# Performance work log

Measured on AMD Instinct MI355X. Metric: run time of the kernel, lower is better.

Reference implementation:

```python
import jax, jax.numpy as jnp
import numpy as np
from jax import lax

EPS = 1e-4  # BatchNorm eps from the module
K = 3       # kernel_size
PAD = 1     # padding


def setup_inputs() -> dict:
    key = jax.random.key(0)
    k1, k2, k3 = jax.random.split(key, 3)
    N, Cin, H, Wd = 32, 256, 56, 56
    Cout = 256
    x = jax.random.normal(k1, (N, Cin, H, Wd), dtype=jnp.float32)
    gamma = jnp.ones((Cin,), dtype=jnp.float32)
    beta_bn = jnp.zeros((Cin,), dtype=jnp.float32)
    W = jax.random.normal(k2, (Cout, Cin, K, K), dtype=jnp.float32) * 0.05
    b = jax.random.normal(k3, (Cout,), dtype=jnp.float32) * 0.01
    return {"x": x, "gamma": gamma, "beta_bn": beta_bn, "W": W, "b": b}


def _conv(x, w, padding):
    return lax.conv_general_dilated(
        x, w, window_strides=(1, 1),
        padding=[(padding, padding), (padding, padding)],
        dimension_numbers=("NCHW", "OIHW", "NCHW"))


def reference(x, gamma, beta_bn, W, b):
    # BatchNorm2d in training mode: batch statistics over (N, H, W), biased var
    mu = jnp.mean(x, axis=(0, 2, 3), keepdims=True)
    var = jnp.var(x, axis=(0, 2, 3), keepdims=True)
    xn = (x - mu) * lax.rsqrt(var + EPS)
    xn = xn * gamma[None, :, None, None] + beta_bn[None, :, None, None]

    # BinActiv: per-pixel channel-mean of |x|, then sign-binarize
    m = jnp.mean(jnp.abs(xn), axis=1, keepdims=True)  # [N,1,H,W]
    xb = jnp.sign(xn)

    # Binarize weights; alpha = L1 norm per output filter / n
    n = W.shape[1] * W.shape[2] * W.shape[3]
    alpha = jnp.sum(jnp.abs(W), axis=(1, 2, 3)) / n  # [Cout]
    Wb = jnp.sign(W)

    y = _conv(xb, Wb, PAD) + b[None, :, None, None]

    # beta map: box filter (stride 1) over channel-mean magnitudes
    box = jnp.full((1, 1, K, K), 1.0 / (K * K), dtype=x.dtype)
    beta_map = _conv(m, box, PAD)  # [N,1,Ho,Wo]

    out = jax.nn.relu(y * beta_map * alpha[None, :, None, None])
    return out
```

## Files before the change

### kernel.cpp

```cpp
#include <hip/hip_runtime.h>
#include <cstdint>
#include <cstddef>

#define N_    32
#define C_    256
#define H_    56
#define W_    56
#define HW_   (H_ * W_)
#define NHW_  (N_ * HW_)
#define COUT_ 256
#define EPS_  1e-4f
#define PW_   58
#define PIMG_ (PW_ * PW_)

__global__ void k_bn_partial(const float* __restrict__ x,
                             float* __restrict__ ps, float* __restrict__ pq) {
    const int c = blockIdx.x >> 3;
    const int s = blockIdx.x & 7;
    const int t = threadIdx.x;
    float sm = 0.f, sq = 0.f;
    for (int n = s * 4; n < s * 4 + 4; ++n) {
        const float4* p = (const float4*)(x + (size_t)(n * C_ + c) * HW_);
        for (int i = t; i < HW_ / 4; i += 256) {
            float4 v = p[i];
            sm += v.x + v.y + v.z + v.w;
            sq += v.x * v.x + v.y * v.y + v.z * v.z + v.w * v.w;
        }
    }
    __shared__ float ls[256], lq[256];
    ls[t] = sm; lq[t] = sq;
    __syncthreads();
    for (int off = 128; off >= 1; off >>= 1) {
        if (t < off) { ls[t] += ls[t + off]; lq[t] += lq[t + off]; }
        __syncthreads();
    }
    if (t == 0) { ps[s * C_ + c] = ls[0]; pq[s * C_ + c] = lq[0]; }
}

__global__ void k_bn_final(const float* __restrict__ ps, const float* __restrict__ pq,
                           const float* __restrict__ gamma, const float* __restrict__ beta,
                           float* __restrict__ a, float* __restrict__ bb) {
    const int c = threadIdx.x;
    float sm = 0.f, sq = 0.f;
    for (int s = 0; s < 8; ++s) { sm += ps[s * C_ + c]; sq += pq[s * C_ + c]; }
    float mu   = sm * (1.f / NHW_);
    float var  = sq * (1.f / NHW_) - mu * mu;
    float rstd = rsqrtf(var + EPS_);
    float g    = gamma[c] * rstd;
    a[c]  = g;
    bb[c] = beta[c] - mu * g;
}

__global__ void k_wpack(const float* __restrict__ Wt, float* __restrict__ alpha,
                        uint64_t* __restrict__ wbits, int* __restrict__ ctab) {
    const int co = blockIdx.x;
    const int ci = threadIdx.x;
    const int lane = ci & 63, wave = ci >> 6;
    const float* p = Wt + (size_t)(co * C_ + ci) * 9;
    float wv[9];
    float asum = 0.f;
#pragma unroll
    for (int t = 0; t < 9; ++t) { wv[t] = p[t]; asum += fabsf(wv[t]); }
    __shared__ int Pl[9];
    if (ci < 9) Pl[ci] = 0;
    __syncthreads();
#pragma unroll
    for (int t = 0; t < 9; ++t) {
        uint64_t mask = __ballot(wv[t] > 0.f);
        if (lane == 0) {
            wbits[((size_t)wave * 9 + t) * COUT_ + co] = mask;
            atomicAdd(&Pl[t], (int)__popcll(mask));
        }
    }
    __shared__ float red[256];
    red[ci] = asum;
    __syncthreads();
    for (int off = 128; off >= 1; off >>= 1) {
        if (ci < off) red[ci] += red[ci + off];
        __syncthreads();
    }
    if (ci == 0) alpha[co] = red[0] * (1.f / 2304.f);
    if (ci < 9) {
        const int rc = ci / 3, cc = ci % 3;
        unsigned m9 = (rc == 0 ? 0x007u : 0u) | (rc == 2 ? 0x1C0u : 0u)
                    | (cc == 0 ? 0x049u : 0u) | (cc == 2 ? 0x124u : 0u);
        int s = 0;
#pragma unroll
        for (int t = 0; t < 9; ++t)
            if ((m9 >> t) & 1) s += 2 * Pl[t] - 256;
        ctab[ci * 256 + co] = s;
    }
}

__global__ void k_mpack(const float* __restrict__ x, const float* __restrict__ a,
                        const float* __restrict__ bb, uint64_t* __restrict__ xbits,
                        float* __restrict__ m) {
    const int p = blockIdx.x * 256 + threadIdx.x;
    const int wd = blockIdx.y;
    const int n = p / HW_;
    const int hw = p - n * HW_;
    const int h = hw / W_;
    const int w = hw - h * W_;
    const float* xp = x + (size_t)n * C_ * HW_ + (size_t)(wd * 64) * HW_ + hw;
    float macc = 0.f;
    uint64_t bw = 0;
#pragma unroll
    for (int j = 0; j < 64; ++j) {
        const int c = wd * 64 + j;
        float xn = fmaf(xp[(size_t)j * HW_], a[c], bb[c]);
        macc += fabsf(xn);
        bw |= (xn > 0.f) ? (1ull << j) : 0ull;
    }
    xbits[((size_t)wd * N_ + n) * PIMG_ + (size_t)(h + 1) * PW_ + (w + 1)] = bw;
    atomicAdd(&m[p], macc * (1.f / C_));
}

__global__ void k_box(const float* __restrict__ m, float* __restrict__ beta_map) {
    const int idx = blockIdx.x * 256 + threadIdx.x;
    if (idx >= NHW_) return;
    const int w = idx % W_;
    const int h = (idx / W_) % H_;
    const int n = idx / HW_;
    const float* mp = m + (size_t)n * HW_;
    float s = 0.f;
#pragma unroll
    for (int dh = 0; dh < 3; ++dh) {
        int ih = h + dh - 1;
        if (ih < 0 || ih >= H_) continue;
#pragma unroll
        for (int dw = 0; dw < 3; ++dw) {
            int iw = w + dw - 1;
            if (iw < 0 || iw >= W_) continue;
            s += mp[ih * W_ + iw];
        }
    }
    beta_map[idx] = s * (1.f / 9.f);
}

#define XNP(ACC, X64, W64) do {                                   \
    uint32_t _wl = (uint32_t)(W64), _wh = (uint32_t)((W64) >> 32); \
    uint32_t _xl = (uint32_t)(X64), _xh = (uint32_t)((X64) >> 32); \
    uint32_t _t0, _t1;                                             \
    asm("v_xor_b32 %0, %3, %5\n\t"                                 \
        "v_xor_b32 %1, %4, %6\n\t"                                 \
        "v_bcnt_u32_b32 %2, %0, %2\n\t"                            \
        "v_bcnt_u32_b32 %2, %1, %2"                                \
        : "=&v"(_t0), "=&v"(_t1), "+v"(ACC)                        \
        : "s"(_wl), "s"(_wh), "v"(_xl), "v"(_xh));                 \
} while (0)

__global__ void __launch_bounds__(256, 8)
k_conv(const uint64_t* __restrict__ xbits, const uint64_t* __restrict__ wbits,
       const int* __restrict__ ctab, const float* __restrict__ beta_map,
       const float* __restrict__ alpha, const float* __restrict__ bias,
       float* __restrict__ out) {
    const int p   = blockIdx.x * 256 + (int)threadIdx.x;
    const int grp = blockIdx.y;
    const int n  = p / HW_;
    const int hw = p - n * HW_;
    const int h  = hw / W_;
    const int w  = hw - h * W_;

    const int rowcls = (h == 0) ? 0 : ((h == H_ - 1) ? 2 : 1);
    const int colcls = (w == 0) ? 0 : ((w == W_ - 1) ? 2 : 1);
    const int* crow = ctab + (rowcls * 3 + colcls) * 256 + grp * 64;
    const float bm = beta_map[p];
    float* op = out + (size_t)n * COUT_ * HW_ + (size_t)(grp * 64) * HW_ + hw;

#pragma unroll 1
    for (int ch = 0; ch < 8; ++ch) {
        int acc[8];
#pragma unroll
        for (int i = 0; i < 8; ++i) acc[i] = 0;

#pragma unroll 1
        for (int wd = 0; wd < 4; ++wd) {
            const uint64_t* xp = xbits + ((size_t)wd * N_ + n) * PIMG_
                                       + (size_t)h * PW_ + w;
            const uint64_t* wq = wbits + (size_t)wd * 9 * COUT_ + grp * 64 + ch * 8;
#pragma unroll 3
            for (int t = 0; t < 9; ++t) {
                const uint64_t xv = *(const volatile uint64_t*)(xp + (t / 3) * PW_ + (t % 3));
                const uint64_t* wr = wq + t * COUT_;
#pragma unroll
                for (int i = 0; i < 8; ++i) XNP(acc[i], xv, wr[i]);
            }
        }

#pragma unroll
        for (int i = 0; i < 8; ++i) {
            const int coi = ch * 8 + i;
            const int co  = grp * 64 + coi;
            const int dot = 2304 - 2 * acc[i] + crow[coi];
            float o = ((float)dot + bias[co]) * bm * alpha[co];
            o = fmaxf(o, 0.f);
            op[(size_t)coi * HW_] = o;
        }
    }
}

extern "C" void kernel_launch(void* const* d_in, const int* in_sizes, int n_in,
                              void* d_out, int out_size, void* d_ws, size_t ws_size,
                              hipStream_t stream) {
    (void)in_sizes; (void)n_in; (void)out_size; (void)ws_size;
    const float* x     = (const float*)d_in[0];
    const float* gamma = (const float*)d_in[1];
    const float* betab = (const float*)d_in[2];
    const float* Wt    = (const float*)d_in[3];
    const float* b     = (const float*)d_in[4];
    float* out = (float*)d_out;

    uint8_t* base = (uint8_t*)d_ws;
    float*    ps       = (float*)(base + 0);
    float*    pq       = (float*)(base + 8192);
    float*    a        = (float*)(base + 16384);
    float*    bb       = (float*)(base + 17408);
    float*    alpha    = (float*)(base + 18432);
    int*      ctab     = (int*)(base + 19456);
    uint64_t* wbits    = (uint64_t*)(base + 28672);
    uint64_t* xbits    = (uint64_t*)(base + 102400);
    float*    m        = (float*)(base + 3547136);
    float*    beta_map = (float*)(base + 3948544);

    k_bn_partial<<<2048, 256, 0, stream>>>(x, ps, pq);
    k_bn_final<<<1, 256, 0, stream>>>(ps, pq, gamma, betab, a, bb);
    k_wpack<<<COUT_, 256, 0, stream>>>(Wt, alpha, wbits, ctab);
    hipMemsetAsync(xbits, 0, (size_t)N_ * PIMG_ * 4 * sizeof(uint64_t), stream);
    hipMemsetAsync(m, 0, (size_t)NHW_ * sizeof(float), stream);
    k_mpack<<<dim3(NHW_ / 256, 4), 256, 0, stream>>>(x, a, bb, xbits, m);
    k_box<<<(NHW_ + 255) / 256, 256, 0, stream>>>(m, beta_map);
    k_conv<<<dim3(NHW_ / 256, 4), 256, 0, stream>>>(xbits, wbits, ctab, beta_map, alpha, b, out);
}
```

Before: 359.5 us.

## Retile binary conv to compute two adjacent pixels by eight channels per thread

```diff
diff --git a/kernel.cpp b/kernel.cpp
--- a/kernel.cpp
+++ b/kernel.cpp
@@ -154,48 +154,57 @@
        const int* __restrict__ ctab, const float* __restrict__ beta_map,
        const float* __restrict__ alpha, const float* __restrict__ bias,
        float* __restrict__ out) {
-    const int p   = blockIdx.x * 256 + (int)threadIdx.x;
+    const int idx = blockIdx.x * 512 + (int)threadIdx.x * 2;
     const int grp = blockIdx.y;
-    const int n  = p / HW_;
-    const int hw = p - n * HW_;
+    const int n  = idx / HW_;
+    const int hw = idx - n * HW_;
     const int h  = hw / W_;
     const int w  = hw - h * W_;
 
-    const int rowcls = (h == 0) ? 0 : ((h == H_ - 1) ? 2 : 1);
-    const int colcls = (w == 0) ? 0 : ((w == W_ - 1) ? 2 : 1);
-    const int* crow = ctab + (rowcls * 3 + colcls) * 256 + grp * 64;
-    const float bm = beta_map[p];
-    float* op = out + (size_t)n * COUT_ * HW_ + (size_t)(grp * 64) * HW_ + hw;
+    int acc0[8], acc1[8];
+#pragma unroll
+    for (int i = 0; i < 8; ++i) { acc0[i] = 0; acc1[i] = 0; }
 
 #pragma unroll 1
-    for (int ch = 0; ch < 8; ++ch) {
-        int acc[8];
-#pragma unroll
-        for (int i = 0; i < 8; ++i) acc[i] = 0;
-
-#pragma unroll 1
-        for (int wd = 0; wd < 4; ++wd) {
-            const uint64_t* xp = xbits + ((size_t)wd * N_ + n) * PIMG_
-                                       + (size_t)h * PW_ + w;
-            const uint64_t* wq = wbits + (size_t)wd * 9 * COUT_ + grp * 64 + ch * 8;
-#pragma unroll 3
-            for (int t = 0; t < 9; ++t) {
-                const uint64_t xv = *(const volatile uint64_t*)(xp + (t / 3) * PW_ + (t % 3));
-                const uint64_t* wr = wq + t * COUT_;
-#pragma unroll
-                for (int i = 0; i < 8; ++i) XNP(acc[i], xv, wr[i]);
+    for (int wd = 0; wd < 4; ++wd) {
+        const uint64_t* xp = xbits + ((size_t)wd * N_ + n) * PIMG_
+                                   + (size_t)h * PW_ + w;
+        const uint64_t* wq = wbits + (size_t)wd * 9 * COUT_ + grp * 8;
+#pragma unroll
+        for (int r = 0; r < 3; ++r) {
+            const ulonglong2* q = (const ulonglong2*)(xp + r * PW_);
+            const ulonglong2 qa = q[0], qb = q[1];
+            const uint64_t xv[4] = { qa.x, qa.y, qb.x, qb.y };
+#pragma unroll
+            for (int c = 0; c < 3; ++c) {
+                const uint64_t* wr = wq + (r * 3 + c) * COUT_;
+#pragma unroll
+                for (int i = 0; i < 8; ++i) {
+                    XNP(acc0[i], xv[c],     wr[i]);
+                    XNP(acc1[i], xv[c + 1], wr[i]);
+                }
             }
         }
-
-#pragma unroll
-        for (int i = 0; i < 8; ++i) {
-            const int coi = ch * 8 + i;
-            const int co  = grp * 64 + coi;
-            const int dot = 2304 - 2 * acc[i] + crow[coi];
-            float o = ((float)dot + bias[co]) * bm * alpha[co];
-            o = fmaxf(o, 0.f);
-            op[(size_t)coi * HW_] = o;
-        }
+    }
+
+    const int rowcls  = (h == 0) ? 0 : ((h == H_ - 1) ? 2 : 1);
+    const int colcls0 = (w == 0) ? 0 : 1;
+    const int colcls1 = (w + 1 == W_ - 1) ? 2 : 1;
+    const int* crow0 = ctab + (rowcls * 3 + colcls0) * 256 + grp * 8;
+    const int* crow1 = ctab + (rowcls * 3 + colcls1) * 256 + grp * 8;
+    const float bm0 = beta_map[idx];
+    const float bm1 = beta_map[idx + 1];
+    float* op = out + (size_t)n * COUT_ * HW_ + (size_t)(grp * 8) * HW_ + hw;
+
+#pragma unroll
+    for (int i = 0; i < 8; ++i) {
+        const int co = grp * 8 + i;
+        const float al = alpha[co], bi = bias[co];
+        const int d0 = 2304 - 2 * acc0[i] + crow0[i];
+        const int d1 = 2304 - 2 * acc1[i] + crow1[i];
+        const float o0 = fmaxf(((float)d0 + bi) * bm0 * al, 0.f);
+        const float o1 = fmaxf(((float)d1 + bi) * bm1 * al, 0.f);
+        *(float2*)(op + (size_t)i * HW_) = make_float2(o0, o1);
     }
 }
 
@@ -229,5 +238,5 @@
     hipMemsetAsync(m, 0, (size_t)NHW_ * sizeof(float), stream);
     k_mpack<<<dim3(NHW_ / 256, 4), 256, 0, stream>>>(x, a, bb, xbits, m);
     k_box<<<(NHW_ + 255) / 256, 256, 0, stream>>>(m, beta_map);
-    k_conv<<<dim3(NHW_ / 256, 4), 256, 0, stream>>>(xbits, wbits, ctab, beta_map, alpha, b, out);
-}
+    k_conv<<<dim3(NHW_ / 512, 32), 256, 0, stream>>>(xbits, wbits, ctab, beta_map, alpha, b, out);
+}
```

New measurement: 299.4 us. -16.7%, faster.
